# Optimization experiments

Measured on AMD Instinct MI355X. Metric: run time of the kernel, lower is better.

The kernel has to match this reference:

```python
import jax, jax.numpy as jnp
import numpy as np


def setup_inputs() -> dict:
    key = jax.random.key(0)
    k1, k2 = jax.random.split(key)
    B, H, S, D = 1, 8, 4096, 64
    CHUNK = 256
    N = S // CHUNK  # 16 chunks
    q = jax.random.normal(k1, (B, H, S, D), dtype=jnp.float32)
    kv_quad_state = jax.random.normal(k2, (B, H, N, D, D, D), dtype=jnp.float32)
    return {"q": q, "kv_quad_state": kv_quad_state}


def reference(q, kv_quad_state):
    # O = 0.5 * einsum('bhndef,bhncd,bhnce->bhncf', S, Q_scaled, Q_scaled)
    # where Q is scaled by head_dim**-0.5 and chunked along seq.
    b, h, s, d = q.shape
    n = kv_quad_state.shape[2]
    c = s // n  # chunk_size
    q_scale = jnp.asarray(d, q.dtype) ** -0.5
    qc = (q * q_scale).reshape(b, h, n, c, d)  # (b,h,n,c,d)
    # pairwise contraction: first Q@S over d -> (b,h,n,c,e,f), then weight by Q_ce, sum e
    tmp = jnp.einsum('bhncd,bhndef->bhncef', qc, kv_quad_state)
    out = 0.5 * jnp.einsum('bhnce,bhncef->bhncf', qc, tmp)
    return out.reshape(b, h, s, d)
```

## Files before the change

kernel.cpp:

```cpp
#include <hip/hip_runtime.h>
#include <hip/hip_fp16.h>

typedef __attribute__((ext_vector_type(4))) float f32x4;
typedef __attribute__((ext_vector_type(8))) _Float16 f16x8;
typedef __attribute__((ext_vector_type(2))) _Float16 f16x2;
typedef __attribute__((ext_vector_type(2))) __fp16 fp16x2_raw;

union F16X8 { f16x2 p[4]; f16x8 w; };

static __device__ __forceinline__ f16x2 pkrtz(float a, float b) {
    fp16x2_raw r = __builtin_amdgcn_cvt_pkrtz(a, b);
    return __builtin_bit_cast(f16x2, r);
}

#define QS 68

#define LOADB(BUF, dd) do {                                           \
    const float* _p = Sb + (size_t)(dd) * 4096;                       \
    _Pragma("unroll") for (int _K = 0; _K < 2; ++_K)                  \
    _Pragma("unroll") for (int _j = 0; _j < 8; ++_j)                  \
        b##BUF[_K][_j] = _p[_K * 2048 + _j * 64];                     \
} while (0)

#define COMPUTE(BUF, dd) do {                                         \
    f16x8 _bb[2];                                                     \
    _Pragma("unroll") for (int _K = 0; _K < 2; ++_K) {                \
        F16X8 _bu;                                                    \
        _Pragma("unroll") for (int _h = 0; _h < 4; ++_h)              \
            _bu.p[_h] = pkrtz(b##BUF[_K][2*_h], b##BUF[_K][2*_h+1]);  \
        _bb[_K] = _bu.w;                                              \
    }                                                                 \
    _Pragma("unroll") for (int _M = 0; _M < 4; ++_M) {                \
        float _sf = qsbase[_M * (16 * QS) + (dd)];                    \
        f16x2 _sh = pkrtz(_sf, _sf);                                  \
        _Pragma("unroll") for (int _K = 0; _K < 2; ++_K) {            \
            F16X8 _au;                                                \
            _Pragma("unroll") for (int _h = 0; _h < 4; ++_h)          \
                _au.p[_h] = _sh * u[_M][_K][_h];                      \
            acc[_M] = __builtin_amdgcn_mfma_f32_16x16x32_f16(_au.w, _bb[_K], acc[_M], 0, 0, 0); \
        }                                                             \
    }                                                                 \
} while (0)

__global__ __launch_bounds__(256, 2) void quad_form_kernel(
    const float* __restrict__ q, const float* __restrict__ kv, float* __restrict__ out)
{
    __shared__ float qs[256 * QS];

    const int tid = threadIdx.x;

    const int wg = blockIdx.x;
    const int xcd = wg & 7, p = wg >> 3;
    const int chunk = xcd * 16 + (p >> 2);
    const int f0 = (p & 3) * 16;

    const int lane = tid & 63;
    const int w = tid >> 6;
    const int ra = lane & 15, kg = lane >> 4;

    const float* qch = q  + (size_t)chunk * 16384;
    const float* Sch = kv + (size_t)chunk * 262144;
    float*       och = out + (size_t)chunk * 16384;

#pragma unroll
    for (int i = 0; i < 16; ++i) {
        int idx4 = i * 256 + tid;
        int row = idx4 >> 4, col = (idx4 & 15) << 2;
        f32x4 v = *(const f32x4*)(qch + idx4 * 4);
        v *= 0.125f;
        *(f32x4*)&qs[row * QS + col] = v;
    }
    __syncthreads();

    const float* Sb = Sch + kg * 512 + f0 + ra;
    const float* qsbase = &qs[(w * 64 + ra) * QS];

    f16x2 u[4][2][4];
#pragma unroll
    for (int Mt = 0; Mt < 4; ++Mt)
#pragma unroll
        for (int Ks = 0; Ks < 2; ++Ks) {
            const float* qr = qsbase + Mt * (16 * QS) + Ks * 32 + kg * 8;
            f32x4 g0 = *(const f32x4*)qr;
            f32x4 g1 = *(const f32x4*)(qr + 4);
            u[Mt][Ks][0] = pkrtz(g0[0], g0[1]);
            u[Mt][Ks][1] = pkrtz(g0[2], g0[3]);
            u[Mt][Ks][2] = pkrtz(g1[0], g1[1]);
            u[Mt][Ks][3] = pkrtz(g1[2], g1[3]);
        }

    f32x4 acc[4] = {};
    float bA[2][8], bB[2][8], bC[2][8];

    LOADB(A, 0); LOADB(B, 1); LOADB(C, 2);

    int i = 0;
#pragma unroll 1
    for (int it = 0; it < 21; ++it) {
        COMPUTE(A, i); if (i + 3 < 64) LOADB(A, i + 3); ++i;
        COMPUTE(B, i); if (i + 3 < 64) LOADB(B, i + 3); ++i;
        COMPUTE(C, i); if (i + 3 < 64) LOADB(C, i + 3); ++i;
    }
    COMPUTE(A, 63);

#pragma unroll
    for (int Mt = 0; Mt < 4; ++Mt)
#pragma unroll
        for (int j = 0; j < 4; ++j)
            och[(w * 64 + Mt * 16 + kg * 4 + j) * 64 + f0 + ra] = 0.5f * acc[Mt][j];
}

extern "C" void kernel_launch(void* const* d_in, const int* in_sizes, int n_in,
                              void* d_out, int out_size, void* d_ws, size_t ws_size,
                              hipStream_t stream) {
    const float* q  = (const float*)d_in[0];
    const float* kv = (const float*)d_in[1];
    float* out = (float*)d_out;
    hipLaunchKernelGGL(quad_form_kernel, dim3(512), dim3(256), 0, stream, q, kv, out);
}
```

Measured before the change: 38.48 us.

## Split each chunk across two workgroups and store scaled Q as fp16 in LDS

```diff
diff --git a/kernel.cpp b/kernel.cpp
--- a/kernel.cpp
+++ b/kernel.cpp
@@ -12,8 +12,12 @@
     fp16x2_raw r = __builtin_amdgcn_cvt_pkrtz(a, b);
     return __builtin_bit_cast(f16x2, r);
 }
+static __device__ __forceinline__ f16x2 splat16(unsigned short s) {
+    unsigned v = (unsigned)s | ((unsigned)s << 16);
+    return __builtin_bit_cast(f16x2, v);
+}
 
-#define QS 68
+#define QS 72
 
 #define LOADB(BUF, dd) do {                                           \
     const float* _p = Sb + (size_t)(dd) * 4096;                       \
@@ -30,9 +34,8 @@
             _bu.p[_h] = pkrtz(b##BUF[_K][2*_h], b##BUF[_K][2*_h+1]);  \
         _bb[_K] = _bu.w;                                              \
     }                                                                 \
-    _Pragma("unroll") for (int _M = 0; _M < 4; ++_M) {                \
-        float _sf = qsbase[_M * (16 * QS) + (dd)];                    \
-        f16x2 _sh = pkrtz(_sf, _sf);                                  \
+    _Pragma("unroll") for (int _M = 0; _M < 2; ++_M) {                \
+        f16x2 _sh = splat16(qs16[qsrow + _M * (16 * QS) + (dd)]);     \
         _Pragma("unroll") for (int _K = 0; _K < 2; ++_K) {            \
             F16X8 _au;                                                \
             _Pragma("unroll") for (int _h = 0; _h < 4; ++_h)          \
@@ -42,54 +45,59 @@
     }                                                                 \
 } while (0)
 
-__global__ __launch_bounds__(256, 2) void quad_form_kernel(
+__global__ __launch_bounds__(256, 4) void quad_form_kernel(
     const float* __restrict__ q, const float* __restrict__ kv, float* __restrict__ out)
 {
-    __shared__ float qs[256 * QS];
+    __shared__ unsigned short qs16[128 * QS];
 
     const int tid = threadIdx.x;
 
     const int wg = blockIdx.x;
-    const int xcd = wg & 7, p = wg >> 3;
-    const int chunk = xcd * 16 + (p >> 2);
-    const int f0 = (p & 3) * 16;
+    const int xcd = wg & 7;
+    const int idx = wg >> 3;
+    const int chunk = xcd * 16 + (idx >> 3);
+    const int sub = idx & 7;
+    const int f0 = (sub >> 1) * 16;
+    const int chalf = sub & 1;
 
     const int lane = tid & 63;
     const int w = tid >> 6;
     const int ra = lane & 15, kg = lane >> 4;
 
-    const float* qch = q  + (size_t)chunk * 16384;
+    const float* qch = q  + (size_t)chunk * 16384 + chalf * 8192;
     const float* Sch = kv + (size_t)chunk * 262144;
-    float*       och = out + (size_t)chunk * 16384;
+    float*       och = out + (size_t)chunk * 16384 + chalf * 8192;
 
 #pragma unroll
-    for (int i = 0; i < 16; ++i) {
+    for (int i = 0; i < 8; ++i) {
         int idx4 = i * 256 + tid;
-        int row = idx4 >> 4, col = (idx4 & 15) << 2;
+        int row = idx4 >> 4, col4 = idx4 & 15;
         f32x4 v = *(const f32x4*)(qch + idx4 * 4);
         v *= 0.125f;
-        *(f32x4*)&qs[row * QS + col] = v;
+        f16x2 h0 = pkrtz(v[0], v[1]);
+        f16x2 h1 = pkrtz(v[2], v[3]);
+        unsigned pair[2] = { __builtin_bit_cast(unsigned, h0),
+                             __builtin_bit_cast(unsigned, h1) };
+        *(unsigned long long*)&qs16[row * QS + col4 * 4] =
+            *(unsigned long long*)pair;
     }
     __syncthreads();
 
     const float* Sb = Sch + kg * 512 + f0 + ra;
-    const float* qsbase = &qs[(w * 64 + ra) * QS];
+    const int qsrow = (w * 32 + ra) * QS;
 
-    f16x2 u[4][2][4];
+    f16x2 u[2][2][4];
 #pragma unroll
-    for (int Mt = 0; Mt < 4; ++Mt)
+    for (int Mt = 0; Mt < 2; ++Mt)
 #pragma unroll
         for (int Ks = 0; Ks < 2; ++Ks) {
-            const float* qr = qsbase + Mt * (16 * QS) + Ks * 32 + kg * 8;
-            f32x4 g0 = *(const f32x4*)qr;
-            f32x4 g1 = *(const f32x4*)(qr + 4);
-            u[Mt][Ks][0] = pkrtz(g0[0], g0[1]);
-            u[Mt][Ks][1] = pkrtz(g0[2], g0[3]);
-            u[Mt][Ks][2] = pkrtz(g1[0], g1[1]);
-            u[Mt][Ks][3] = pkrtz(g1[2], g1[3]);
+            F16X8 t;
+            t.w = *(const f16x8*)&qs16[qsrow + Mt * (16 * QS) + Ks * 32 + kg * 8];
+#pragma unroll
+            for (int h = 0; h < 4; ++h) u[Mt][Ks][h] = t.p[h];
         }
 
-    f32x4 acc[4] = {};
+    f32x4 acc[2] = {};
     float bA[2][8], bB[2][8], bC[2][8];
 
     LOADB(A, 0); LOADB(B, 1); LOADB(C, 2);
@@ -104,10 +112,10 @@
     COMPUTE(A, 63);
 
 #pragma unroll
-    for (int Mt = 0; Mt < 4; ++Mt)
+    for (int Mt = 0; Mt < 2; ++Mt)
 #pragma unroll
         for (int j = 0; j < 4; ++j)
-            och[(w * 64 + Mt * 16 + kg * 4 + j) * 64 + f0 + ra] = 0.5f * acc[Mt][j];
+            och[(w * 32 + Mt * 16 + kg * 4 + j) * 64 + f0 + ra] = 0.5f * acc[Mt][j];
 }
 
 extern "C" void kernel_launch(void* const* d_in, const int* in_sizes, int n_in,
@@ -116,5 +124,5 @@
     const float* q  = (const float*)d_in[0];
     const float* kv = (const float*)d_in[1];
     float* out = (float*)d_out;
-    hipLaunchKernelGGL(quad_form_kernel, dim3(512), dim3(256), 0, stream, q, kv, out);
+    hipLaunchKernelGGL(quad_form_kernel, dim3(1024), dim3(256), 0, stream, q, kv, out);
 }
```

After: 60.26 us. 56.6% more time.

## Stream state slabs into an LDS ring via async global-to-LDS loads

Applied to the files above, without the earlier changes.

```diff
diff --git a/kernel.cpp b/kernel.cpp
--- a/kernel.cpp
+++ b/kernel.cpp
@@ -5,6 +5,7 @@
 typedef __attribute__((ext_vector_type(8))) _Float16 f16x8;
 typedef __attribute__((ext_vector_type(2))) _Float16 f16x2;
 typedef __attribute__((ext_vector_type(2))) __fp16 fp16x2_raw;
+typedef unsigned u32;
 
 union F16X8 { f16x2 p[4]; f16x8 w; };
 
@@ -12,40 +13,25 @@
     fp16x2_raw r = __builtin_amdgcn_cvt_pkrtz(a, b);
     return __builtin_bit_cast(f16x2, r);
 }
+static __device__ __forceinline__ f16x2 splat16(unsigned short s) {
+    unsigned v = (unsigned)s | ((unsigned)s << 16);
+    return __builtin_bit_cast(f16x2, v);
+}
+static __device__ __forceinline__ void gl_lds16(const float* g, float* l) {
+    __builtin_amdgcn_global_load_lds(
+        (const __attribute__((address_space(1))) u32*)g,
+        (__attribute__((address_space(3))) u32*)l, 16, 0, 0);
+}
 
-#define QS 68
-
-#define LOADB(BUF, dd) do {                                           \
-    const float* _p = Sb + (size_t)(dd) * 4096;                       \
-    _Pragma("unroll") for (int _K = 0; _K < 2; ++_K)                  \
-    _Pragma("unroll") for (int _j = 0; _j < 8; ++_j)                  \
-        b##BUF[_K][_j] = _p[_K * 2048 + _j * 64];                     \
-} while (0)
-
-#define COMPUTE(BUF, dd) do {                                         \
-    f16x8 _bb[2];                                                     \
-    _Pragma("unroll") for (int _K = 0; _K < 2; ++_K) {                \
-        F16X8 _bu;                                                    \
-        _Pragma("unroll") for (int _h = 0; _h < 4; ++_h)              \
-            _bu.p[_h] = pkrtz(b##BUF[_K][2*_h], b##BUF[_K][2*_h+1]);  \
-        _bb[_K] = _bu.w;                                              \
-    }                                                                 \
-    _Pragma("unroll") for (int _M = 0; _M < 4; ++_M) {                \
-        float _sf = qsbase[_M * (16 * QS) + (dd)];                    \
-        f16x2 _sh = pkrtz(_sf, _sf);                                  \
-        _Pragma("unroll") for (int _K = 0; _K < 2; ++_K) {            \
-            F16X8 _au;                                                \
-            _Pragma("unroll") for (int _h = 0; _h < 4; ++_h)          \
-                _au.p[_h] = _sh * u[_M][_K][_h];                      \
-            acc[_M] = __builtin_amdgcn_mfma_f32_16x16x32_f16(_au.w, _bb[_K], acc[_M], 0, 0, 0); \
-        }                                                             \
-    }                                                                 \
-} while (0)
+#define QS 72
+#define RING 10
+#define DEPTH 9
 
 __global__ __launch_bounds__(256, 2) void quad_form_kernel(
     const float* __restrict__ q, const float* __restrict__ kv, float* __restrict__ out)
 {
-    __shared__ float qs[256 * QS];
+    __shared__ __align__(16) unsigned short qs16[256 * QS];
+    __shared__ __align__(16) float ring[RING * 1024];
 
     const int tid = threadIdx.x;
 
@@ -65,43 +51,83 @@
 #pragma unroll
     for (int i = 0; i < 16; ++i) {
         int idx4 = i * 256 + tid;
-        int row = idx4 >> 4, col = (idx4 & 15) << 2;
+        int row = idx4 >> 4, col4 = idx4 & 15;
         f32x4 v = *(const f32x4*)(qch + idx4 * 4);
         v *= 0.125f;
-        *(f32x4*)&qs[row * QS + col] = v;
+        f16x2 h0 = pkrtz(v[0], v[1]);
+        f16x2 h1 = pkrtz(v[2], v[3]);
+        unsigned pair[2] = { __builtin_bit_cast(unsigned, h0),
+                             __builtin_bit_cast(unsigned, h1) };
+        *(unsigned long long*)&qs16[row * QS + col4 * 4] = *(unsigned long long*)pair;
     }
     __syncthreads();
 
-    const float* Sb = Sch + kg * 512 + f0 + ra;
-    const float* qsbase = &qs[(w * 64 + ra) * QS];
+    const float* Sg = Sch + f0 + (size_t)((w * 16 + (lane >> 2)) * 64 + ((lane & 3) << 2));
+    float* ringw = &ring[0] + w * 256;
+    const float* ringr = &ring[0] + kg * 128 + ra;
+    const int qsrow = (w * 64 + ra) * QS;
 
     f16x2 u[4][2][4];
 #pragma unroll
     for (int Mt = 0; Mt < 4; ++Mt)
 #pragma unroll
         for (int Ks = 0; Ks < 2; ++Ks) {
-            const float* qr = qsbase + Mt * (16 * QS) + Ks * 32 + kg * 8;
-            f32x4 g0 = *(const f32x4*)qr;
-            f32x4 g1 = *(const f32x4*)(qr + 4);
-            u[Mt][Ks][0] = pkrtz(g0[0], g0[1]);
-            u[Mt][Ks][1] = pkrtz(g0[2], g0[3]);
-            u[Mt][Ks][2] = pkrtz(g1[0], g1[1]);
-            u[Mt][Ks][3] = pkrtz(g1[2], g1[3]);
+            F16X8 t;
+            t.w = *(const f16x8*)&qs16[qsrow + Mt * (16 * QS) + Ks * 32 + kg * 8];
+#pragma unroll
+            for (int h = 0; h < 4; ++h) u[Mt][Ks][h] = t.p[h];
         }
 
     f32x4 acc[4] = {};
-    float bA[2][8], bB[2][8], bC[2][8];
 
-    LOADB(A, 0); LOADB(B, 1); LOADB(C, 2);
+    auto compute = [&](unsigned roff, int d) {
+        const float* bl = ringr + roff;
+        f16x8 bb[2];
+#pragma unroll
+        for (int K = 0; K < 2; ++K) {
+            F16X8 bu;
+#pragma unroll
+            for (int h = 0; h < 4; ++h)
+                bu.p[h] = pkrtz(bl[K * 512 + (2 * h) * 16], bl[K * 512 + (2 * h + 1) * 16]);
+            bb[K] = bu.w;
+        }
+#pragma unroll
+        for (int Mt = 0; Mt < 4; ++Mt) {
+            f16x2 sh = splat16(qs16[qsrow + Mt * (16 * QS) + d]);
+#pragma unroll
+            for (int K = 0; K < 2; ++K) {
+                F16X8 au;
+#pragma unroll
+                for (int h = 0; h < 4; ++h) au.p[h] = sh * u[Mt][K][h];
+                acc[Mt] = __builtin_amdgcn_mfma_f32_16x16x32_f16(au.w, bb[K], acc[Mt], 0, 0, 0);
+            }
+        }
+    };
 
-    int i = 0;
+#pragma unroll
+    for (int s = 0; s < DEPTH; ++s)
+        gl_lds16(Sg + (size_t)s * 4096, ringw + s * 1024);
+
+    unsigned ro = 0, wo = DEPTH * 1024;
 #pragma unroll 1
-    for (int it = 0; it < 21; ++it) {
-        COMPUTE(A, i); if (i + 3 < 64) LOADB(A, i + 3); ++i;
-        COMPUTE(B, i); if (i + 3 < 64) LOADB(B, i + 3); ++i;
-        COMPUTE(C, i); if (i + 3 < 64) LOADB(C, i + 3); ++i;
+    for (int i = 0; i < 64 - DEPTH; ++i) {
+        asm volatile("s_waitcnt vmcnt(8)" ::: "memory");
+        __builtin_amdgcn_s_barrier();
+        asm volatile("" ::: "memory");
+        gl_lds16(Sg + (size_t)(i + DEPTH) * 4096, ringw + wo);
+        compute(ro, i);
+        ro += 1024; if (ro == RING * 1024) ro = 0;
+        wo += 1024; if (wo == RING * 1024) wo = 0;
     }
-    COMPUTE(A, 63);
+
+    asm volatile("s_waitcnt vmcnt(0)" ::: "memory");
+    __builtin_amdgcn_s_barrier();
+    asm volatile("" ::: "memory");
+#pragma unroll 1
+    for (int i = 64 - DEPTH; i < 64; ++i) {
+        compute(ro, i);
+        ro += 1024; if (ro == RING * 1024) ro = 0;
+    }
 
 #pragma unroll
     for (int Mt = 0; Mt < 4; ++Mt)
```

After: 47.22 us. 22.7% more time.
